# Performance work log

Measured on AMD Instinct MI355X. Metric: run time of the kernel, lower is better.

The kernel has to match this reference:

```python
import jax, jax.numpy as jnp
import numpy as np

B, S, D_IN, D_OUT = 4, 2048, 4096, 11008


def setup_inputs() -> dict:
    key = jax.random.key(0)
    kx, kw, ks, kb = jax.random.split(key, 4)
    x = jax.random.normal(kx, (B, S, D_IN), dtype=jnp.float32)
    # Simulate fp8 storage: values are exactly representable in float8_e4m3fn.
    w_raw = jax.random.normal(kw, (D_OUT, D_IN), dtype=jnp.float32)
    w_q = w_raw.astype(jnp.float8_e4m3fn).astype(jnp.float32)
    # Per-output-channel dequant scale (positive).
    scale = jax.random.uniform(ks, (D_OUT, 1), dtype=jnp.float32, minval=0.01, maxval=0.1)
    bias = jax.random.normal(kb, (D_OUT,), dtype=jnp.float32)
    return {"x": x, "w_q": w_q, "scale": scale, "bias": bias}


def reference(x, w_q, scale, bias):
    # dequantize_tensor: fp8 payload * per-channel scale -> full-precision weight [D_OUT, D_IN]
    w = w_q * scale
    # F.linear(x, w, bias) = x @ w.T + bias
    out = jnp.einsum('bsd,od->bso', x, w) + bias
    return out
```

## Files before the change

kernel.cpp:

```cpp
#include <hip/hip_runtime.h>
#include <hip/hip_bf16.h>
#include <stdint.h>

#define M_DIM 8192
#define N_DIM 11008
#define K_DIM 4096
#define BM 128
#define BN 128
#define BK 32

typedef __bf16 bf16_8 __attribute__((ext_vector_type(8)));
typedef float f32x4 __attribute__((ext_vector_type(4)));

__device__ __forceinline__ uint32_t pack_bf2(float lo, float hi) {
    uint32_t ulo = __float_as_uint(lo);
    uint32_t uhi = __float_as_uint(hi);
    ulo = (ulo + 0x7fffu + ((ulo >> 16) & 1u)) >> 16;
    uhi = (uhi + 0x7fffu + ((uhi >> 16) & 1u)) >> 16;
    return ulo | (uhi << 16);
}

__global__ __launch_bounds__(256) void cvt_f32_bf16(const float* __restrict__ src,
                                                    uint2* __restrict__ dst, int n4) {
    int i = blockIdx.x * 256 + threadIdx.x;
    if (i >= n4) return;
    float4 a = ((const float4*)src)[i];
    uint2 o;
    o.x = pack_bf2(a.x, a.y);
    o.y = pack_bf2(a.z, a.w);
    dst[i] = o;
}

__device__ __forceinline__ void load_lds16(const __bf16* g, __bf16* l) {
    __builtin_amdgcn_global_load_lds(
        (__attribute__((address_space(1))) void*)(g),
        (__attribute__((address_space(3))) void*)(l),
        16, 0, 0);
}

__global__ __launch_bounds__(256) void gemm_bt_scaled(
    const __bf16* __restrict__ A, const __bf16* __restrict__ W,
    const float* __restrict__ scale, const float* __restrict__ bias,
    float* __restrict__ C) {
    __shared__ __align__(16) __bf16 As[BM * BK];
    __shared__ __align__(16) __bf16 Bs[BN * BK];

    const int t = threadIdx.x;
    const int wave = t >> 6;
    const int lane = t & 63;
    const int wm = wave >> 1;
    const int wn = wave & 1;

    const int m0 = blockIdx.y * BM;
    const int n0 = blockIdx.x * BN;

    const int srow = lane >> 2;
    const int skk = ((lane & 3) ^ ((lane >> 3) & 3)) * 8;

    const __bf16* Ag = A + (long)(m0 + wave * 16 + srow) * K_DIM + skk;
    const __bf16* Wg = W + (long)(n0 + wave * 16 + srow) * K_DIM + skk;
    __bf16* AsW = &As[(wave * 16) * BK];
    __bf16* BsW = &Bs[(wave * 16) * BK];

    f32x4 acc[4][4] = {};

    const int lrow = lane & 15;
    const int swz = (lrow >> 1) & 3;
    const int lk = ((lane >> 4) ^ swz) * 8;

    for (int k0 = 0; k0 < K_DIM; k0 += BK) {
        __syncthreads();
        load_lds16(Ag + k0, AsW);
        load_lds16(Ag + (long)64 * K_DIM + k0, AsW + 64 * BK);
        load_lds16(Wg + k0, BsW);
        load_lds16(Wg + (long)64 * K_DIM + k0, BsW + 64 * BK);
        __syncthreads();

        bf16_8 af[4], bfr[4];
#pragma unroll
        for (int i = 0; i < 4; i++)
            af[i] = *(const bf16_8*)&As[(wm * 64 + i * 16 + lrow) * BK + lk];
#pragma unroll
        for (int j = 0; j < 4; j++)
            bfr[j] = *(const bf16_8*)&Bs[(wn * 64 + j * 16 + lrow) * BK + lk];
#pragma unroll
        for (int i = 0; i < 4; i++)
#pragma unroll
            for (int j = 0; j < 4; j++)
                acc[i][j] = __builtin_amdgcn_mfma_f32_16x16x32_bf16(af[i], bfr[j], acc[i][j], 0, 0, 0);
    }

    const int crow4 = (lane >> 4) * 4;
    const int ccol = lane & 15;
#pragma unroll
    for (int j = 0; j < 4; j++) {
        const int n = n0 + wn * 64 + j * 16 + ccol;
        const float sc = scale[n];
        const float bi = bias[n];
#pragma unroll
        for (int i = 0; i < 4; i++) {
            const int mbase = m0 + wm * 64 + i * 16 + crow4;
#pragma unroll
            for (int r = 0; r < 4; r++) {
                C[(long)(mbase + r) * N_DIM + n] = acc[i][j][r] * sc + bi;
            }
        }
    }
}

extern "C" void kernel_launch(void* const* d_in, const int* in_sizes, int n_in,
                              void* d_out, int out_size, void* d_ws, size_t ws_size,
                              hipStream_t stream) {
    const float* x = (const float*)d_in[0];
    const float* w_q = (const float*)d_in[1];
    const float* scale = (const float*)d_in[2];
    const float* bias = (const float*)d_in[3];
    float* out = (float*)d_out;

    __bf16* x_bf = (__bf16*)d_ws;
    __bf16* w_bf = (__bf16*)((char*)d_ws + (size_t)M_DIM * K_DIM * sizeof(__bf16));

    const int n4x = (M_DIM * K_DIM) / 4;
    const int n4w = (N_DIM * K_DIM) / 4;
    cvt_f32_bf16<<<(n4x + 255) / 256, 256, 0, stream>>>(x, (uint2*)x_bf, n4x);
    cvt_f32_bf16<<<(n4w + 255) / 256, 256, 0, stream>>>(w_q, (uint2*)w_bf, n4w);

    dim3 grid(N_DIM / BN, M_DIM / BM);
    gemm_bt_scaled<<<grid, 256, 0, stream>>>(x_bf, w_bf, scale, bias, out);
}
```

Before: 1.455 ms.

## Use 256x256 tiles with 4-stage LDS pipeline and XCD-aware block swizzle

Grows the block tile to 256x256 with 8 waves and gives each wave 8x4 MFMA tiles. Global-to-LDS loads are issued three stages ahead through a 4-deep ring buffer, with vmcnt waits and a single barrier per step. Block ids are remapped so that neighbouring tiles land on the same XCD, which should improve L2 reuse. The changes target exposed load latency, double barriers and low arithmetic intensity, at the cost of higher register and LDS use that may lower occupancy.

Measured after the change: 1.533 ms. 5.4% more time.

```diff
diff --git a/kernel.cpp b/kernel.cpp
--- a/kernel.cpp
+++ b/kernel.cpp
@@ -5,9 +5,14 @@
 #define M_DIM 8192
 #define N_DIM 11008
 #define K_DIM 4096
-#define BM 128
-#define BN 128
+#define BM 256
+#define BN 256
 #define BK 32
+#define NT (K_DIM / BK)
+#define NBX (N_DIM / BN)
+#define NBY (M_DIM / BM)
+#define NBLK (NBX * NBY)
+#define CPX (NBLK / 8)
 
 typedef __bf16 bf16_8 __attribute__((ext_vector_type(8)));
 typedef float f32x4 __attribute__((ext_vector_type(4)));
@@ -38,57 +43,100 @@
         16, 0, 0);
 }
 
-__global__ __launch_bounds__(256) void gemm_bt_scaled(
+#define VMCNT(n) asm volatile("s_waitcnt vmcnt(" #n ")" ::: "memory")
+#define CFENCE asm volatile("" ::: "memory")
+
+__device__ __forceinline__ void wg_barrier() {
+    CFENCE;
+    __builtin_amdgcn_s_barrier();
+    CFENCE;
+}
+
+__device__ __forceinline__ void stage_tile(const __bf16* Ag, const __bf16* Wg,
+                                           __bf16* Asl, __bf16* Bsl,
+                                           int wave, long ko) {
+    __bf16* la = Asl + wave * 16 * BK;
+    __bf16* lb = Bsl + wave * 16 * BK;
+    load_lds16(Ag + ko, la);
+    load_lds16(Ag + 128 * (long)K_DIM + ko, la + 128 * BK);
+    load_lds16(Wg + ko, lb);
+    load_lds16(Wg + 128 * (long)K_DIM + ko, lb + 128 * BK);
+}
+
+__device__ __forceinline__ void compute_step(const __bf16* __restrict__ Abase,
+                                             const __bf16* __restrict__ Bbase,
+                                             f32x4 (&acc)[8][4]) {
+    bf16_8 af[8], bv[4];
+#pragma unroll
+    for (int i = 0; i < 8; i++) af[i] = *(const bf16_8*)(Abase + i * 16 * BK);
+#pragma unroll
+    for (int j = 0; j < 4; j++) bv[j] = *(const bf16_8*)(Bbase + j * 16 * BK);
+    __builtin_amdgcn_s_setprio(1);
+#pragma unroll
+    for (int i = 0; i < 8; i++)
+#pragma unroll
+        for (int j = 0; j < 4; j++)
+            acc[i][j] = __builtin_amdgcn_mfma_f32_16x16x32_bf16(af[i], bv[j], acc[i][j], 0, 0, 0);
+    __builtin_amdgcn_s_setprio(0);
+}
+
+__global__ __launch_bounds__(512, 2) void gemm_bt_scaled(
     const __bf16* __restrict__ A, const __bf16* __restrict__ W,
     const float* __restrict__ scale, const float* __restrict__ bias,
     float* __restrict__ C) {
-    __shared__ __align__(16) __bf16 As[BM * BK];
-    __shared__ __align__(16) __bf16 Bs[BN * BK];
+    __shared__ __align__(16) __bf16 As[4][BM * BK];
+    __shared__ __align__(16) __bf16 Bs[4][BN * BK];
 
     const int t = threadIdx.x;
     const int wave = t >> 6;
     const int lane = t & 63;
-    const int wm = wave >> 1;
-    const int wn = wave & 1;
+    const int wm = wave >> 2;
+    const int wn = wave & 3;
 
-    const int m0 = blockIdx.y * BM;
-    const int n0 = blockIdx.x * BN;
+    const int bid = (int)blockIdx.x;
+    const int swz = (bid & 7) * CPX + (bid >> 3);
+    const int by = swz / NBX;
+    const int bx = swz - by * NBX;
+    const int m0 = by * BM;
+    const int n0 = bx * BN;
 
     const int srow = lane >> 2;
-    const int skk = ((lane & 3) ^ ((lane >> 3) & 3)) * 8;
-
-    const __bf16* Ag = A + (long)(m0 + wave * 16 + srow) * K_DIM + skk;
-    const __bf16* Wg = W + (long)(n0 + wave * 16 + srow) * K_DIM + skk;
-    __bf16* AsW = &As[(wave * 16) * BK];
-    __bf16* BsW = &Bs[(wave * 16) * BK];
-
-    f32x4 acc[4][4] = {};
+    const int sch = ((lane & 3) ^ ((lane >> 3) & 3)) * 8;
+    const __bf16* Ag = A + (long)(m0 + wave * 16 + srow) * K_DIM + sch;
+    const __bf16* Wg = W + (long)(n0 + wave * 16 + srow) * K_DIM + sch;
 
     const int lrow = lane & 15;
-    const int swz = (lrow >> 1) & 3;
-    const int lk = ((lane >> 4) ^ swz) * 8;
+    const int swzr = (lrow >> 1) & 3;
+    const int lk = ((lane >> 4) ^ swzr) * 8;
+    const int aoff = (wm * 128 + lrow) * BK + lk;
+    const int boff = (wn * 64 + lrow) * BK + lk;
 
-    for (int k0 = 0; k0 < K_DIM; k0 += BK) {
-        __syncthreads();
-        load_lds16(Ag + k0, AsW);
-        load_lds16(Ag + (long)64 * K_DIM + k0, AsW + 64 * BK);
-        load_lds16(Wg + k0, BsW);
-        load_lds16(Wg + (long)64 * K_DIM + k0, BsW + 64 * BK);
-        __syncthreads();
+    f32x4 acc[8][4] = {};
 
-        bf16_8 af[4], bfr[4];
-#pragma unroll
-        for (int i = 0; i < 4; i++)
-            af[i] = *(const bf16_8*)&As[(wm * 64 + i * 16 + lrow) * BK + lk];
-#pragma unroll
-        for (int j = 0; j < 4; j++)
-            bfr[j] = *(const bf16_8*)&Bs[(wn * 64 + j * 16 + lrow) * BK + lk];
-#pragma unroll
-        for (int i = 0; i < 4; i++)
-#pragma unroll
-            for (int j = 0; j < 4; j++)
-                acc[i][j] = __builtin_amdgcn_mfma_f32_16x16x32_bf16(af[i], bfr[j], acc[i][j], 0, 0, 0);
+    stage_tile(Ag, Wg, &As[0][0], &Bs[0][0], wave, 0);
+    stage_tile(Ag, Wg, &As[1][0], &Bs[1][0], wave, (long)BK);
+    stage_tile(Ag, Wg, &As[2][0], &Bs[2][0], wave, 2L * BK);
+    VMCNT(8);
+    wg_barrier();
+
+    int tt = 0;
+    for (; tt < NT - 3; ++tt) {
+        const int sl = tt & 3;
+        const int sn = (tt + 3) & 3;
+        stage_tile(Ag, Wg, &As[sn][0], &Bs[sn][0], wave, (long)(tt + 3) * BK);
+        compute_step(&As[sl][aoff], &Bs[sl][boff], acc);
+        VMCNT(8);
+        wg_barrier();
     }
+    compute_step(&As[tt & 3][aoff], &Bs[tt & 3][boff], acc);
+    VMCNT(4);
+    wg_barrier();
+    ++tt;
+    compute_step(&As[tt & 3][aoff], &Bs[tt & 3][boff], acc);
+    VMCNT(0);
+    wg_barrier();
+    ++tt;
+    compute_step(&As[tt & 3][aoff], &Bs[tt & 3][boff], acc);
 
     const int crow4 = (lane >> 4) * 4;
     const int ccol = lane & 15;
@@ -98,8 +146,8 @@
         const float sc = scale[n];
         const float bi = bias[n];
 #pragma unroll
-        for (int i = 0; i < 4; i++) {
-            const int mbase = m0 + wm * 64 + i * 16 + crow4;
+        for (int i = 0; i < 8; i++) {
+            const int mbase = m0 + wm * 128 + i * 16 + crow4;
 #pragma unroll
             for (int r = 0; r < 4; r++) {
                 C[(long)(mbase + r) * N_DIM + n] = acc[i][j][r] * sc + bi;
@@ -125,6 +173,5 @@
     cvt_f32_bf16<<<(n4x + 255) / 256, 256, 0, stream>>>(x, (uint2*)x_bf, n4x);
     cvt_f32_bf16<<<(n4w + 255) / 256, 256, 0, stream>>>(w_q, (uint2*)w_bf, n4w);
 
-    dim3 grid(N_DIM / BN, M_DIM / BM);
-    gemm_bt_scaled<<<grid, 256, 0, stream>>>(x_bf, w_bf, scale, bias, out);
+    gemm_bt_scaled<<<dim3(NBLK), 512, 0, stream>>>(x_bf, w_bf, scale, bias, out);
 }
```
